# Performance work log

Hardware: AMD Instinct MI355X
Metric: run time of the kernel (lower is better)

The kernel has to match this reference:

```python
import jax, jax.numpy as jnp
import numpy as np

B, L, H, E = 2, 2048, 16, 64

def setup_inputs() -> dict:
    key = jax.random.key(0)
    kq, kk, kv = jax.random.split(key, 3)
    queries = jax.random.normal(kq, (B, L, H, E), dtype=jnp.float32)
    keys = jax.random.normal(kk, (B, L, H, E), dtype=jnp.float32)
    values = jax.random.normal(kv, (B, L, H, E), dtype=jnp.float32)
    # causal mask: True above the diagonal gets masked out (as in torch.triu(..., diagonal=1))
    attn_mask = jnp.broadcast_to(
        jnp.triu(jnp.ones((L, L), dtype=bool), k=1)[None, None, :, :], (B, 1, L, L)
    )
    return {"queries": queries, "keys": keys, "values": values, "attn_mask": attn_mask}

def reference(queries, keys, values, attn_mask):
    Ef = queries.shape[-1]
    # scores: [B, H, L, S]
    scores = jnp.einsum('blhe,bshe->bhls', queries, keys)
    scores = jnp.where(attn_mask, -jnp.inf, scores)
    # FAITHFUL to source: scale = 1/sqrt(E), then scores * (1.0/scale) = scores * sqrt(E)
    scale = 1.0 / jnp.sqrt(jnp.float32(Ef))
    attention_weights = jax.nn.softmax(scores * (1.0 / scale), axis=-1)
    # dropout p = 0.0 -> identity
    V = jnp.einsum('bhls,bshe->blhe', attention_weights, values)
    return V
```

## Files before the change

### kernel.cpp

```cpp
#include <hip/hip_runtime.h>

#define Bb 2
#define Ls 2048
#define Hh 16
#define Ee 64

#define QT 128
#define KT 64
#define BUFB 24576

typedef __fp16 f16;
typedef __attribute__((ext_vector_type(2)))  __fp16 f16x2;
typedef __attribute__((ext_vector_type(8)))  __fp16 f16x8;
typedef __attribute__((ext_vector_type(16))) float  f32x16;

union Frag  { f16x8 v; f16x2 h[4]; unsigned int u[4]; };
union U32H2 { f16x2 h; unsigned int u; };

__device__ __forceinline__ f16x2 pkrtz(float a, float b) {
  return __builtin_amdgcn_cvt_pkrtz(a, b);
}
__device__ __forceinline__ f32x16 mfma16(f16x8 a, f16x8 b, f32x16 c) {
  return __builtin_amdgcn_mfma_f32_32x32x16_f16(a, b, c, 0, 0, 0);
}
__device__ __forceinline__ f32x16 zero16() {
  f32x16 z;
#pragma unroll
  for (int i = 0; i < 16; ++i) z[i] = 0.f;
  return z;
}

#define SC 11.541560327111707f

__launch_bounds__(256, 2)
__global__ void fattn(const float* __restrict__ Q, const float* __restrict__ K,
                      const float* __restrict__ V, float* __restrict__ O) {
  __shared__ __align__(16) char lds[2 * BUFB];

  const int tid  = threadIdx.x;
  const int lane = tid & 63;
  const int wid  = tid >> 6;
  const int h2   = lane >> 5;
  const int qc   = lane & 31;
  const int bid  = blockIdx.x;

  const int bh  = bid & 31;
  const int qtx = bid >> 5;
  const int qt  = (qtx < 8) ? qtx : 23 - qtx;
  const int b   = bh >> 4;
  const int h   = bh & 15;

  const int q0   = qt * QT;
  const int q0w  = q0 + wid * 32;
  const int qrow = q0w + qc;

  f16x8 qh[4], ql[4];
  {
    const float* qp = Q + (((size_t)(b * Ls + qrow) * Hh) + h) * Ee + h2 * 8;
#pragma unroll
    for (int c = 0; c < 4; ++c) {
      float x[8];
      *(float4*)&x[0] = *(const float4*)(qp + c * 16);
      *(float4*)&x[4] = *(const float4*)(qp + c * 16 + 4);
      Frag fh, fl;
#pragma unroll
      for (int j = 0; j < 4; ++j) {
        f16x2 hi = pkrtz(x[2 * j], x[2 * j + 1]);
        fl.h[j] = pkrtz(x[2 * j] - (float)hi[0], x[2 * j + 1] - (float)hi[1]);
        fh.h[j] = hi;
      }
      qh[c] = fh.v;
      ql[c] = fl.v;
    }
  }

  const int r    = tid >> 2;
  const int cbe  = (tid & 3) * 16;
  const int kv0  = (tid & 31) * 2;
  const int ec   = tid >> 5;
  const float* kp0 = K + (((size_t)(b * Ls + r) * Hh) + h) * Ee + cbe;
  const float* vp0 = V + (((size_t)(b * Ls + kv0) * Hh) + h) * Ee + ec * 8;
  const int rowstride = Hh * Ee;

  float4 ka0, ka1, ka2, ka3, va0, va1, vb0, vb1;

#define STAGE_LOAD(KB)                                              \
  {                                                                 \
    const float* kp = kp0 + (size_t)(KB) * rowstride;               \
    ka0 = *(const float4*)(kp);                                     \
    ka1 = *(const float4*)(kp + 4);                                 \
    ka2 = *(const float4*)(kp + 8);                                 \
    ka3 = *(const float4*)(kp + 12);                                \
    const float* vp = vp0 + (size_t)(KB) * rowstride;               \
    va0 = *(const float4*)(vp);                                     \
    va1 = *(const float4*)(vp + 4);                                 \
    vb0 = *(const float4*)(vp + rowstride);                         \
    vb1 = *(const float4*)(vp + rowstride + 4);                     \
  }

#define STAGE_WRITE(BUF)                                            \
  {                                                                 \
    char* Khi = (BUF);                                              \
    char* Klo = (BUF) + 8192;                                       \
    char* Vt  = (BUF) + 16384;                                      \
    float x[16];                                                    \
    *(float4*)&x[0]  = ka0; *(float4*)&x[4]  = ka1;                 \
    *(float4*)&x[8]  = ka2; *(float4*)&x[12] = ka3;                 \
    Frag fh0, fl0, fh1, fl1;                                        \
    _Pragma("unroll")                                               \
    for (int j = 0; j < 4; ++j) {                                   \
      f16x2 hi0 = pkrtz(x[2 * j], x[2 * j + 1]);                    \
      fl0.h[j] = pkrtz(x[2 * j] - (float)hi0[0],                    \
                       x[2 * j + 1] - (float)hi0[1]);               \
      fh0.h[j] = hi0;                                               \
      f16x2 hi1 = pkrtz(x[8 + 2 * j], x[8 + 2 * j + 1]);            \
      fl1.h[j] = pkrtz(x[8 + 2 * j] - (float)hi1[0],                \
                       x[8 + 2 * j + 1] - (float)hi1[1]);           \
      fh1.h[j] = hi1;                                               \
    }                                                               \
    const int sw = (r & 7) << 4;                                    \
    char* dh = Khi + r * 128;                                       \
    char* dl = Klo + r * 128;                                       \
    *(f16x8*)(dh + ((cbe * 2) ^ sw))      = fh0.v;                  \
    *(f16x8*)(dh + ((cbe * 2 + 16) ^ sw)) = fh1.v;                  \
    *(f16x8*)(dl + ((cbe * 2) ^ sw))      = fl0.v;                  \
    *(f16x8*)(dl + ((cbe * 2 + 16) ^ sw)) = fl1.v;                  \
    float y0[8], y1[8];                                             \
    *(float4*)&y0[0] = va0; *(float4*)&y0[4] = va1;                 \
    *(float4*)&y1[0] = vb0; *(float4*)&y1[4] = vb1;                 \
    _Pragma("unroll")                                               \
    for (int j = 0; j < 8; ++j) {                                   \
      U32H2 pr;                                                     \
      pr.h = pkrtz(y0[j], y1[j]);                                   \
      const int e = ec * 8 + j;                                     \
      *(unsigned int*)(Vt + e * 128 + ((kv0 * 2) ^ ((e & 7) << 4))) = pr.u; \
    }                                                               \
  }

  f32x16 o0 = zero16(), o1 = zero16();
  float m = -3.0e38f, l = 0.f;

  const int NT = (q0 + QT) / KT;

  STAGE_LOAD(0);
  STAGE_WRITE(lds);
  __syncthreads();
  int cur = 0;

  for (int t = 0; t < NT; ++t) {
    const int kb = t * KT;
    const bool pf = (t + 1 < NT);
    if (pf) STAGE_LOAD(kb + KT);

    if (kb <= q0w + 31) {
      char* bufc = lds + cur * BUFB;
      char* Khi = bufc;
      char* Klo = bufc + 8192;
      char* Vt  = bufc + 16384;

      f32x16 s0, s1;
      {
        const int sw = (qc & 7) << 4;
        const char* kbh0 = Khi + qc * 128;
        const char* kbl0 = Klo + qc * 128;
        const char* kbh1 = Khi + (32 + qc) * 128;
        const char* kbl1 = Klo + (32 + qc) * 128;
        f32x16 a0h = zero16(), a0l = zero16(), a1h = zero16(), a1l = zero16();
        __builtin_amdgcn_s_setprio(1);
#pragma unroll
        for (int c = 0; c < 4; ++c) {
          const int off = ((c << 5) + (h2 << 4)) ^ sw;
          f16x8 ah0 = *(const f16x8*)(kbh0 + off);
          f16x8 al0 = *(const f16x8*)(kbl0 + off);
          f16x8 ah1 = *(const f16x8*)(kbh1 + off);
          f16x8 al1 = *(const f16x8*)(kbl1 + off);
          a0h = mfma16(ah0, qh[c], a0h);
          a1h = mfma16(ah1, qh[c], a1h);
          a0l = mfma16(ah0, ql[c], a0l);
          a1l = mfma16(ah1, ql[c], a1l);
          a0l = mfma16(al0, qh[c], a0l);
          a1l = mfma16(al1, qh[c], a1l);
        }
        __builtin_amdgcn_s_setprio(0);
#pragma unroll
        for (int i = 0; i < 16; ++i) { s0[i] = a0h[i] + a0l[i]; s1[i] = a1h[i] + a1l[i]; }
      }

      float p[32];
#pragma unroll
      for (int rr = 0; rr < 16; ++rr) { p[rr] = s0[rr]; p[16 + rr] = s1[rr]; }

      if (kb + KT - 1 > q0w) {
#pragma unroll
        for (int st = 0; st < 2; ++st)
#pragma unroll
          for (int rr = 0; rr < 16; ++rr) {
            const int kv = kb + st * 32 + ((rr & 3) + 8 * (rr >> 2) + 4 * h2);
            if (kv > qrow) p[st * 16 + rr] = -3.0e38f;
          }
      }

      float w[16];
#pragma unroll
      for (int i = 0; i < 16; ++i) w[i] = fmaxf(p[i], p[i + 16]);
#pragma unroll
      for (int i = 0; i < 8; ++i) w[i] = fmaxf(w[i], w[i + 8]);
#pragma unroll
      for (int i = 0; i < 4; ++i) w[i] = fmaxf(w[i], w[i + 4]);
      w[0] = fmaxf(fmaxf(w[0], w[1]), fmaxf(w[2], w[3]));
      float tm = fmaxf(w[0], __shfl_xor(w[0], 32));

      if (__any(tm > m + 1.0f)) {
        const float mnew = fmaxf(m, tm);
        const float corr = __builtin_amdgcn_exp2f((m - mnew) * SC);
        l *= corr;
#pragma unroll
        for (int rr = 0; rr < 16; ++rr) {
          const float cr = __shfl(corr, (rr & 3) + 8 * (rr >> 2) + 4 * h2);
          o0[rr] *= cr;
          o1[rr] *= cr;
        }
        m = mnew;
      }
      const float base = m * SC;
#pragma unroll
      for (int i = 0; i < 32; ++i) p[i] = __builtin_amdgcn_exp2f(p[i] * SC - base);
      float z[16];
#pragma unroll
      for (int i = 0; i < 16; ++i) z[i] = p[i] + p[i + 16];
#pragma unroll
      for (int i = 0; i < 8; ++i) z[i] += z[i + 8];
#pragma unroll
      for (int i = 0; i < 4; ++i) z[i] += z[i + 4];
      float ps = (z[0] + z[1]) + (z[2] + z[3]);
      ps += __shfl_xor(ps, 32);
      l += ps;

      f16x8 pa[4];
#pragma unroll
      for (int st = 0; st < 2; ++st) {
        unsigned u[8];
#pragma unroll
        for (int g = 0; g < 4; ++g) {
          U32H2 a, bb;
          a.h  = pkrtz(p[st * 16 + 4 * g],     p[st * 16 + 4 * g + 1]);
          bb.h = pkrtz(p[st * 16 + 4 * g + 2], p[st * 16 + 4 * g + 3]);
          u[2 * g]     = a.u;
          u[2 * g + 1] = bb.u;
        }
#pragma unroll
        for (int cp = 0; cp < 2; ++cp) {
          const unsigned ua0 = u[4 * cp], ua1 = u[4 * cp + 1];
          const unsigned ub0 = u[4 * cp + 2], ub1 = u[4 * cp + 3];
          const unsigned t0 = (unsigned)__shfl_xor((int)(h2 ? ua0 : ub0), 32);
          const unsigned t1 = (unsigned)__shfl_xor((int)(h2 ? ua1 : ub1), 32);
          Frag f;
          f.u[0] = h2 ? t0 : ua0;
          f.u[1] = h2 ? t1 : ua1;
          f.u[2] = h2 ? ub0 : t0;
          f.u[3] = h2 ? ub1 : t1;
          pa[st * 2 + cp] = f.v;
        }
      }

      {
        const int sw = (qc & 7) << 4;
        __builtin_amdgcn_s_setprio(1);
#pragma unroll
        for (int c = 0; c < 4; ++c) {
          const int off = ((c << 5) + (h2 << 4)) ^ sw;
          const f16x8 vbl0 = *(const f16x8*)(Vt + (qc)      * 128 + off);
          const f16x8 vbl1 = *(const f16x8*)(Vt + (32 + qc) * 128 + off);
          o0 = mfma16(pa[c], vbl0, o0);
          o1 = mfma16(pa[c], vbl1, o1);
        }
        __builtin_amdgcn_s_setprio(0);
      }
    }

    if (pf) STAGE_WRITE(lds + (cur ^ 1) * BUFB);
    __syncthreads();
    cur ^= 1;
  }

  const float inv = 1.0f / l;
#pragma unroll
  for (int rr = 0; rr < 16; ++rr) {
    const int row = (rr & 3) + 8 * (rr >> 2) + 4 * h2;
    const float iv = __shfl(inv, row);
    float* op = O + (((size_t)(b * Ls + q0w + row) * Hh) + h) * Ee;
    op[qc]      = o0[rr] * iv;
    op[32 + qc] = o1[rr] * iv;
  }
}

extern "C" void kernel_launch(void* const* d_in, const int* in_sizes, int n_in,
                              void* d_out, int out_size, void* d_ws, size_t ws_size,
                              hipStream_t stream) {
  const float* Q = (const float*)d_in[0];
  const float* K = (const float*)d_in[1];
  const float* V = (const float*)d_in[2];
  float* O = (float*)d_out;
  (void)in_sizes; (void)n_in; (void)out_size; (void)d_ws; (void)ws_size;
  dim3 grid(Bb * Hh * (Ls / QT));
  fattn<<<grid, dim3(256), 0, stream>>>(Q, K, V, O);
}
```

Measured before the change: 164.8 us.

## Switch to 16x16x32 MFMA tiles with 8 waves of 16 query rows

```diff
diff --git a/kernel.cpp b/kernel.cpp
--- a/kernel.cpp
+++ b/kernel.cpp
@@ -10,9 +10,9 @@
 #define BUFB 24576
 
 typedef __fp16 f16;
-typedef __attribute__((ext_vector_type(2)))  __fp16 f16x2;
-typedef __attribute__((ext_vector_type(8)))  __fp16 f16x8;
-typedef __attribute__((ext_vector_type(16))) float  f32x16;
+typedef __attribute__((ext_vector_type(2))) __fp16 f16x2;
+typedef __attribute__((ext_vector_type(8))) __fp16 f16x8;
+typedef __attribute__((ext_vector_type(4))) float  f32x4;
 
 union Frag  { f16x8 v; f16x2 h[4]; unsigned int u[4]; };
 union U32H2 { f16x2 h; unsigned int u; };
@@ -20,19 +20,13 @@
 __device__ __forceinline__ f16x2 pkrtz(float a, float b) {
   return __builtin_amdgcn_cvt_pkrtz(a, b);
 }
-__device__ __forceinline__ f32x16 mfma16(f16x8 a, f16x8 b, f32x16 c) {
-  return __builtin_amdgcn_mfma_f32_32x32x16_f16(a, b, c, 0, 0, 0);
-}
-__device__ __forceinline__ f32x16 zero16() {
-  f32x16 z;
-#pragma unroll
-  for (int i = 0; i < 16; ++i) z[i] = 0.f;
-  return z;
+__device__ __forceinline__ f32x4 mfma16(f16x8 a, f16x8 b, f32x4 c) {
+  return __builtin_amdgcn_mfma_f32_16x16x32_f16(a, b, c, 0, 0, 0);
 }
 
 #define SC 11.541560327111707f
 
-__launch_bounds__(256, 2)
+__launch_bounds__(512, 4)
 __global__ void fattn(const float* __restrict__ Q, const float* __restrict__ K,
                       const float* __restrict__ V, float* __restrict__ O) {
   __shared__ __align__(16) char lds[2 * BUFB];
@@ -40,8 +34,8 @@
   const int tid  = threadIdx.x;
   const int lane = tid & 63;
   const int wid  = tid >> 6;
-  const int h2   = lane >> 5;
-  const int qc   = lane & 31;
+  const int g    = lane >> 4;
+  const int q15  = lane & 15;
   const int bid  = blockIdx.x;
 
   const int bh  = bid & 31;
@@ -51,17 +45,17 @@
   const int h   = bh & 15;
 
   const int q0   = qt * QT;
-  const int q0w  = q0 + wid * 32;
-  const int qrow = q0w + qc;
-
-  f16x8 qh[4], ql[4];
+  const int q0w  = q0 + wid * 16;
+  const int qrow = q0w + q15;
+
+  f16x8 qh[2], ql[2];
   {
-    const float* qp = Q + (((size_t)(b * Ls + qrow) * Hh) + h) * Ee + h2 * 8;
-#pragma unroll
-    for (int c = 0; c < 4; ++c) {
+    const float* qp = Q + (((size_t)(b * Ls + qrow) * Hh) + h) * Ee + 8 * g;
+#pragma unroll
+    for (int c = 0; c < 2; ++c) {
       float x[8];
-      *(float4*)&x[0] = *(const float4*)(qp + c * 16);
-      *(float4*)&x[4] = *(const float4*)(qp + c * 16 + 4);
+      *(float4*)&x[0] = *(const float4*)(qp + 32 * c);
+      *(float4*)&x[4] = *(const float4*)(qp + 32 * c + 4);
       Frag fh, fl;
 #pragma unroll
       for (int j = 0; j < 4; ++j) {
@@ -74,208 +68,189 @@
     }
   }
 
-  const int r    = tid >> 2;
-  const int cbe  = (tid & 3) * 16;
+  const int r    = tid >> 3;
+  const int cbe  = (tid & 7) * 8;
   const int kv0  = (tid & 31) * 2;
-  const int ec   = tid >> 5;
+  const int ec4  = (tid >> 5) * 4;
   const float* kp0 = K + (((size_t)(b * Ls + r) * Hh) + h) * Ee + cbe;
-  const float* vp0 = V + (((size_t)(b * Ls + kv0) * Hh) + h) * Ee + ec * 8;
+  const float* vp0 = V + (((size_t)(b * Ls + kv0) * Hh) + h) * Ee + ec4;
   const int rowstride = Hh * Ee;
 
-  float4 ka0, ka1, ka2, ka3, va0, va1, vb0, vb1;
-
-#define STAGE_LOAD(KB)                                              \
-  {                                                                 \
-    const float* kp = kp0 + (size_t)(KB) * rowstride;               \
-    ka0 = *(const float4*)(kp);                                     \
-    ka1 = *(const float4*)(kp + 4);                                 \
-    ka2 = *(const float4*)(kp + 8);                                 \
-    ka3 = *(const float4*)(kp + 12);                                \
-    const float* vp = vp0 + (size_t)(KB) * rowstride;               \
-    va0 = *(const float4*)(vp);                                     \
-    va1 = *(const float4*)(vp + 4);                                 \
-    vb0 = *(const float4*)(vp + rowstride);                         \
-    vb1 = *(const float4*)(vp + rowstride + 4);                     \
-  }
-
-#define STAGE_WRITE(BUF)                                            \
-  {                                                                 \
-    char* Khi = (BUF);                                              \
-    char* Klo = (BUF) + 8192;                                       \
-    char* Vt  = (BUF) + 16384;                                      \
-    float x[16];                                                    \
-    *(float4*)&x[0]  = ka0; *(float4*)&x[4]  = ka1;                 \
-    *(float4*)&x[8]  = ka2; *(float4*)&x[12] = ka3;                 \
-    Frag fh0, fl0, fh1, fl1;                                        \
-    _Pragma("unroll")                                               \
-    for (int j = 0; j < 4; ++j) {                                   \
-      f16x2 hi0 = pkrtz(x[2 * j], x[2 * j + 1]);                    \
-      fl0.h[j] = pkrtz(x[2 * j] - (float)hi0[0],                    \
-                       x[2 * j + 1] - (float)hi0[1]);               \
-      fh0.h[j] = hi0;                                               \
-      f16x2 hi1 = pkrtz(x[8 + 2 * j], x[8 + 2 * j + 1]);            \
-      fl1.h[j] = pkrtz(x[8 + 2 * j] - (float)hi1[0],                \
-                       x[8 + 2 * j + 1] - (float)hi1[1]);           \
-      fh1.h[j] = hi1;                                               \
-    }                                                               \
-    const int sw = (r & 7) << 4;                                    \
-    char* dh = Khi + r * 128;                                       \
-    char* dl = Klo + r * 128;                                       \
-    *(f16x8*)(dh + ((cbe * 2) ^ sw))      = fh0.v;                  \
-    *(f16x8*)(dh + ((cbe * 2 + 16) ^ sw)) = fh1.v;                  \
-    *(f16x8*)(dl + ((cbe * 2) ^ sw))      = fl0.v;                  \
-    *(f16x8*)(dl + ((cbe * 2 + 16) ^ sw)) = fl1.v;                  \
-    float y0[8], y1[8];                                             \
-    *(float4*)&y0[0] = va0; *(float4*)&y0[4] = va1;                 \
-    *(float4*)&y1[0] = vb0; *(float4*)&y1[4] = vb1;                 \
-    _Pragma("unroll")                                               \
-    for (int j = 0; j < 8; ++j) {                                   \
-      U32H2 pr;                                                     \
-      pr.h = pkrtz(y0[j], y1[j]);                                   \
-      const int e = ec * 8 + j;                                     \
+  float4 ka0, ka1, va0, vb0;
+
+#define STAGE_LOAD(KB)                                          \
+  {                                                             \
+    const float* kp = kp0 + (size_t)(KB) * rowstride;           \
+    ka0 = *(const float4*)(kp);                                 \
+    ka1 = *(const float4*)(kp + 4);                             \
+    const float* vp = vp0 + (size_t)(KB) * rowstride;           \
+    va0 = *(const float4*)(vp);                                 \
+    vb0 = *(const float4*)(vp + rowstride);                     \
+  }
+
+#define STAGE_WRITE(BUF)                                        \
+  {                                                             \
+    char* Khi = (BUF);                                          \
+    char* Klo = (BUF) + 8192;                                   \
+    char* Vt  = (BUF) + 16384;                                  \
+    float x[8];                                                 \
+    *(float4*)&x[0] = ka0; *(float4*)&x[4] = ka1;               \
+    Frag fh, fl;                                                \
+    _Pragma("unroll")                                           \
+    for (int j = 0; j < 4; ++j) {                               \
+      f16x2 hi = pkrtz(x[2 * j], x[2 * j + 1]);                 \
+      fl.h[j] = pkrtz(x[2 * j] - (float)hi[0],                  \
+                      x[2 * j + 1] - (float)hi[1]);             \
+      fh.h[j] = hi;                                             \
+    }                                                           \
+    const int sw = (r & 7) << 4;                                \
+    *(f16x8*)(Khi + r * 128 + ((cbe * 2) ^ sw)) = fh.v;         \
+    *(f16x8*)(Klo + r * 128 + ((cbe * 2) ^ sw)) = fl.v;         \
+    _Pragma("unroll")                                           \
+    for (int j = 0; j < 4; ++j) {                               \
+      U32H2 pr;                                                 \
+      pr.h = pkrtz(va0[j], vb0[j]);                             \
+      const int e = ec4 + j;                                    \
       *(unsigned int*)(Vt + e * 128 + ((kv0 * 2) ^ ((e & 7) << 4))) = pr.u; \
-    }                                                               \
-  }
-
-  f32x16 o0 = zero16(), o1 = zero16();
+    }                                                           \
+  }
+
+  f32x4 o0, o1, o2, o3;
+#pragma unroll
+  for (int i = 0; i < 4; ++i) { o0[i] = 0.f; o1[i] = 0.f; o2[i] = 0.f; o3[i] = 0.f; }
   float m = -3.0e38f, l = 0.f;
 
-  const int NT = (q0 + QT) / KT;
+  const int NT = 2 * (qt + 1);
 
   STAGE_LOAD(0);
   STAGE_WRITE(lds);
   __syncthreads();
   int cur = 0;
 
+  const int swr   = (q15 & 7) << 4;
+  const int srcA  = q15 + ((g & 1) ? 32 : 0);
+  const int srcB  = srcA + 16;
+  const int srel  = g >> 1;
+  const int lbase = lane & 48;
+
   for (int t = 0; t < NT; ++t) {
     const int kb = t * KT;
     const bool pf = (t + 1 < NT);
     if (pf) STAGE_LOAD(kb + KT);
 
-    if (kb <= q0w + 31) {
+    if (kb <= q0w + 15) {
       char* bufc = lds + cur * BUFB;
       char* Khi = bufc;
       char* Klo = bufc + 8192;
       char* Vt  = bufc + 16384;
 
-      f32x16 s0, s1;
-      {
-        const int sw = (qc & 7) << 4;
-        const char* kbh0 = Khi + qc * 128;
-        const char* kbl0 = Klo + qc * 128;
-        const char* kbh1 = Khi + (32 + qc) * 128;
-        const char* kbl1 = Klo + (32 + qc) * 128;
-        f32x16 a0h = zero16(), a0l = zero16(), a1h = zero16(), a1l = zero16();
-        __builtin_amdgcn_s_setprio(1);
-#pragma unroll
-        for (int c = 0; c < 4; ++c) {
-          const int off = ((c << 5) + (h2 << 4)) ^ sw;
-          f16x8 ah0 = *(const f16x8*)(kbh0 + off);
-          f16x8 al0 = *(const f16x8*)(kbl0 + off);
-          f16x8 ah1 = *(const f16x8*)(kbh1 + off);
-          f16x8 al1 = *(const f16x8*)(kbl1 + off);
-          a0h = mfma16(ah0, qh[c], a0h);
-          a1h = mfma16(ah1, qh[c], a1h);
-          a0l = mfma16(ah0, ql[c], a0l);
-          a1l = mfma16(ah1, ql[c], a1l);
-          a0l = mfma16(al0, qh[c], a0l);
-          a1l = mfma16(al1, qh[c], a1l);
+      f32x4 p4[4];
+      __builtin_amdgcn_s_setprio(1);
+#pragma unroll
+      for (int st = 0; st < 4; ++st) {
+        const char* kh = Khi + (16 * st + q15) * 128;
+        const char* kl = Klo + (16 * st + q15) * 128;
+        f32x4 acch, accl;
+#pragma unroll
+        for (int i = 0; i < 4; ++i) { acch[i] = 0.f; accl[i] = 0.f; }
+#pragma unroll
+        for (int c = 0; c < 2; ++c) {
+          const int off = ((c << 6) + (g << 4)) ^ swr;
+          f16x8 ah = *(const f16x8*)(kh + off);
+          f16x8 al = *(const f16x8*)(kl + off);
+          acch = mfma16(ah, qh[c], acch);
+          accl = mfma16(ah, ql[c], accl);
+          accl = mfma16(al, qh[c], accl);
         }
-        __builtin_amdgcn_s_setprio(0);
-#pragma unroll
-        for (int i = 0; i < 16; ++i) { s0[i] = a0h[i] + a0l[i]; s1[i] = a1h[i] + a1l[i]; }
-      }
-
-      float p[32];
-#pragma unroll
-      for (int rr = 0; rr < 16; ++rr) { p[rr] = s0[rr]; p[16 + rr] = s1[rr]; }
+        p4[st] = acch + accl;
+      }
+      __builtin_amdgcn_s_setprio(0);
 
       if (kb + KT - 1 > q0w) {
 #pragma unroll
-        for (int st = 0; st < 2; ++st)
-#pragma unroll
-          for (int rr = 0; rr < 16; ++rr) {
-            const int kv = kb + st * 32 + ((rr & 3) + 8 * (rr >> 2) + 4 * h2);
-            if (kv > qrow) p[st * 16 + rr] = -3.0e38f;
+        for (int st = 0; st < 4; ++st)
+#pragma unroll
+          for (int rg = 0; rg < 4; ++rg) {
+            const int kv = kb + 16 * st + 4 * g + rg;
+            if (kv > qrow) p4[st][rg] = -3.0e38f;
           }
       }
 
-      float w[16];
-#pragma unroll
-      for (int i = 0; i < 16; ++i) w[i] = fmaxf(p[i], p[i + 16]);
-#pragma unroll
-      for (int i = 0; i < 8; ++i) w[i] = fmaxf(w[i], w[i + 8]);
-#pragma unroll
-      for (int i = 0; i < 4; ++i) w[i] = fmaxf(w[i], w[i + 4]);
-      w[0] = fmaxf(fmaxf(w[0], w[1]), fmaxf(w[2], w[3]));
-      float tm = fmaxf(w[0], __shfl_xor(w[0], 32));
+      f32x4 tv = p4[0];
+#pragma unroll
+      for (int i = 0; i < 4; ++i) tv[i] = fmaxf(fmaxf(p4[0][i], p4[1][i]), fmaxf(p4[2][i], p4[3][i]));
+      float tm = fmaxf(fmaxf(tv[0], tv[1]), fmaxf(tv[2], tv[3]));
+      tm = fmaxf(tm, __shfl_xor(tm, 16));
+      tm = fmaxf(tm, __shfl_xor(tm, 32));
 
       if (__any(tm > m + 1.0f)) {
         const float mnew = fmaxf(m, tm);
         const float corr = __builtin_amdgcn_exp2f((m - mnew) * SC);
         l *= corr;
 #pragma unroll
-        for (int rr = 0; rr < 16; ++rr) {
-          const float cr = __shfl(corr, (rr & 3) + 8 * (rr >> 2) + 4 * h2);
-          o0[rr] *= cr;
-          o1[rr] *= cr;
+        for (int rg = 0; rg < 4; ++rg) {
+          const float cr = __shfl(corr, lbase | (4 * g + rg));
+          o0[rg] *= cr; o1[rg] *= cr; o2[rg] *= cr; o3[rg] *= cr;
         }
         m = mnew;
       }
       const float base = m * SC;
 #pragma unroll
-      for (int i = 0; i < 32; ++i) p[i] = __builtin_amdgcn_exp2f(p[i] * SC - base);
-      float z[16];
-#pragma unroll
-      for (int i = 0; i < 16; ++i) z[i] = p[i] + p[i + 16];
-#pragma unroll
-      for (int i = 0; i < 8; ++i) z[i] += z[i + 8];
-#pragma unroll
-      for (int i = 0; i < 4; ++i) z[i] += z[i + 4];
-      float ps = (z[0] + z[1]) + (z[2] + z[3]);
-      ps += __shfl_xor(ps, 32);
-      l += ps;
-
-      f16x8 pa[4];
-#pragma unroll
-      for (int st = 0; st < 2; ++st) {
-        unsigned u[8];
-#pragma unroll
-        for (int g = 0; g < 4; ++g) {
-          U32H2 a, bb;
-          a.h  = pkrtz(p[st * 16 + 4 * g],     p[st * 16 + 4 * g + 1]);
-          bb.h = pkrtz(p[st * 16 + 4 * g + 2], p[st * 16 + 4 * g + 3]);
-          u[2 * g]     = a.u;
-          u[2 * g + 1] = bb.u;
-        }
-#pragma unroll
-        for (int cp = 0; cp < 2; ++cp) {
-          const unsigned ua0 = u[4 * cp], ua1 = u[4 * cp + 1];
-          const unsigned ub0 = u[4 * cp + 2], ub1 = u[4 * cp + 3];
-          const unsigned t0 = (unsigned)__shfl_xor((int)(h2 ? ua0 : ub0), 32);
-          const unsigned t1 = (unsigned)__shfl_xor((int)(h2 ? ua1 : ub1), 32);
-          Frag f;
-          f.u[0] = h2 ? t0 : ua0;
-          f.u[1] = h2 ? t1 : ua1;
-          f.u[2] = h2 ? ub0 : t0;
-          f.u[3] = h2 ? ub1 : t1;
-          pa[st * 2 + cp] = f.v;
-        }
-      }
+      for (int st = 0; st < 4; ++st)
+#pragma unroll
+        for (int rg = 0; rg < 4; ++rg)
+          p4[st][rg] = __builtin_amdgcn_exp2f(p4[st][rg] * SC - base);
 
       {
-        const int sw = (qc & 7) << 4;
-        __builtin_amdgcn_s_setprio(1);
-#pragma unroll
-        for (int c = 0; c < 4; ++c) {
-          const int off = ((c << 5) + (h2 << 4)) ^ sw;
-          const f16x8 vbl0 = *(const f16x8*)(Vt + (qc)      * 128 + off);
-          const f16x8 vbl1 = *(const f16x8*)(Vt + (32 + qc) * 128 + off);
-          o0 = mfma16(pa[c], vbl0, o0);
-          o1 = mfma16(pa[c], vbl1, o1);
-        }
-        __builtin_amdgcn_s_setprio(0);
-      }
+        f32x4 sv = (p4[0] + p4[1]) + (p4[2] + p4[3]);
+        float ps = (sv[0] + sv[1]) + (sv[2] + sv[3]);
+        ps += __shfl_xor(ps, 16);
+        ps += __shfl_xor(ps, 32);
+        l += ps;
+      }
+
+      unsigned int u[8];
+#pragma unroll
+      for (int st = 0; st < 4; ++st) {
+        U32H2 w0, w1;
+        w0.h = pkrtz(p4[st][0], p4[st][1]);
+        w1.h = pkrtz(p4[st][2], p4[st][3]);
+        u[2 * st]     = w0.u;
+        u[2 * st + 1] = w1.u;
+      }
+      f16x8 pa[2];
+#pragma unroll
+      for (int c = 0; c < 2; ++c) {
+        const unsigned a0 = (unsigned)__shfl((int)u[4 * c + 0], srcA);
+        const unsigned a1 = (unsigned)__shfl((int)u[4 * c + 1], srcA);
+        const unsigned a2 = (unsigned)__shfl((int)u[4 * c + 0], srcB);
+        const unsigned a3 = (unsigned)__shfl((int)u[4 * c + 1], srcB);
+        const unsigned b0 = (unsigned)__shfl((int)u[4 * c + 2], srcA);
+        const unsigned b1 = (unsigned)__shfl((int)u[4 * c + 3], srcA);
+        const unsigned b2 = (unsigned)__shfl((int)u[4 * c + 2], srcB);
+        const unsigned b3 = (unsigned)__shfl((int)u[4 * c + 3], srcB);
+        Frag f;
+        f.u[0] = srel ? b0 : a0;
+        f.u[1] = srel ? b1 : a1;
+        f.u[2] = srel ? b2 : a2;
+        f.u[3] = srel ? b3 : a3;
+        pa[c] = f.v;
+      }
+
+      __builtin_amdgcn_s_setprio(1);
+#pragma unroll
+      for (int c = 0; c < 2; ++c) {
+        const int coff = ((c << 6) + (g << 4)) ^ swr;
+        const f16x8 v0 = *(const f16x8*)(Vt + (q15)      * 128 + coff);
+        const f16x8 v1 = *(const f16x8*)(Vt + (16 + q15) * 128 + coff);
+        const f16x8 v2 = *(const f16x8*)(Vt + (32 + q15) * 128 + coff);
+        const f16x8 v3 = *(const f16x8*)(Vt + (48 + q15) * 128 + coff);
+        o0 = mfma16(pa[c], v0, o0);
+        o1 = mfma16(pa[c], v1, o1);
+        o2 = mfma16(pa[c], v2, o2);
+        o3 = mfma16(pa[c], v3, o3);
+      }
+      __builtin_amdgcn_s_setprio(0);
     }
 
     if (pf) STAGE_WRITE(lds + (cur ^ 1) * BUFB);
@@ -285,12 +260,13 @@
 
   const float inv = 1.0f / l;
 #pragma unroll
-  for (int rr = 0; rr < 16; ++rr) {
-    const int row = (rr & 3) + 8 * (rr >> 2) + 4 * h2;
-    const float iv = __shfl(inv, row);
-    float* op = O + (((size_t)(b * Ls + q0w + row) * Hh) + h) * Ee;
-    op[qc]      = o0[rr] * iv;
-    op[32 + qc] = o1[rr] * iv;
+  for (int rg = 0; rg < 4; ++rg) {
+    const float iv = __shfl(inv, lbase | (4 * g + rg));
+    float* op = O + (((size_t)(b * Ls + q0w + 4 * g + rg) * Hh) + h) * Ee + q15;
+    op[0]  = o0[rg] * iv;
+    op[16] = o1[rg] * iv;
+    op[32] = o2[rg] * iv;
+    op[48] = o3[rg] * iv;
   }
 }
 
@@ -302,6 +278,5 @@
   const float* V = (const float*)d_in[2];
   float* O = (float*)d_out;
   (void)in_sizes; (void)n_in; (void)out_size; (void)d_ws; (void)ws_size;
-  dim3 grid(Bb * Hh * (Ls / QT));
-  fattn<<<grid, dim3(256), 0, stream>>>(Q, K, V, O);
-}
+  fattn<<<dim3(Bb * Hh * (Ls / QT)), dim3(512), 0, stream>>>(Q, K, V, O);
+}
```

New measurement: 164.3 us. About the same (-0.3%).

## Software-pipeline QK^T one tile ahead and transpose PV output layout

Applied to the files above, without the earlier changes.

```diff
diff --git a/kernel.cpp b/kernel.cpp
--- a/kernel.cpp
+++ b/kernel.cpp
@@ -10,8 +10,8 @@
 #define BUFB 24576
 
 typedef __fp16 f16;
-typedef __attribute__((ext_vector_type(2)))  __fp16 f16x2;
-typedef __attribute__((ext_vector_type(8)))  __fp16 f16x8;
+typedef __attribute__((ext_vector_type(2))) __fp16 f16x2;
+typedef __attribute__((ext_vector_type(8))) __fp16 f16x8;
 typedef __attribute__((ext_vector_type(16))) float  f32x16;
 
 union Frag  { f16x8 v; f16x2 h[4]; unsigned int u[4]; };
@@ -20,7 +20,7 @@
 __device__ __forceinline__ f16x2 pkrtz(float a, float b) {
   return __builtin_amdgcn_cvt_pkrtz(a, b);
 }
-__device__ __forceinline__ f32x16 mfma16(f16x8 a, f16x8 b, f32x16 c) {
+__device__ __forceinline__ f32x16 mfma32(f16x8 a, f16x8 b, f32x16 c) {
   return __builtin_amdgcn_mfma_f32_32x32x16_f16(a, b, c, 0, 0, 0);
 }
 __device__ __forceinline__ f32x16 zero16() {
@@ -31,6 +31,28 @@
 }
 
 #define SC 11.541560327111707f
+
+#define QKT(BUF, S0, S1)                                          \
+  {                                                               \
+    const char* Khi_ = (BUF);                                     \
+    const char* Klo_ = (BUF) + 8192;                              \
+    _Pragma("unroll")                                             \
+    for (int st_ = 0; st_ < 2; ++st_) {                           \
+      const char* kh_ = Khi_ + (32 * st_ + qc) * 128;             \
+      const char* kl_ = Klo_ + (32 * st_ + qc) * 128;             \
+      f32x16 acch_ = zero16(), accl_ = zero16();                  \
+      _Pragma("unroll")                                           \
+      for (int c_ = 0; c_ < 4; ++c_) {                            \
+        const int off_ = ((c_ << 5) + (h2 << 4)) ^ swr;           \
+        f16x8 ah_ = *(const f16x8*)(kh_ + off_);                  \
+        f16x8 al_ = *(const f16x8*)(kl_ + off_);                  \
+        acch_ = mfma32(ah_, qh[c_], acch_);                       \
+        accl_ = mfma32(ah_, ql[c_], accl_);                       \
+        accl_ = mfma32(al_, qh[c_], accl_);                       \
+      }                                                           \
+      if (st_) S1 = acch_ + accl_; else S0 = acch_ + accl_;       \
+    }                                                             \
+  }
 
 __launch_bounds__(256, 2)
 __global__ void fattn(const float* __restrict__ Q, const float* __restrict__ K,
@@ -53,6 +75,7 @@
   const int q0   = qt * QT;
   const int q0w  = q0 + wid * 32;
   const int qrow = q0w + qc;
+  const int swr  = (qc & 7) << 4;
 
   f16x8 qh[4], ql[4];
   {
@@ -140,157 +163,128 @@
   f32x16 o0 = zero16(), o1 = zero16();
   float m = -3.0e38f, l = 0.f;
 
-  const int NT = (q0 + QT) / KT;
+  const int NT = 2 * (qt + 1);
 
   STAGE_LOAD(0);
   STAGE_WRITE(lds);
   __syncthreads();
-  int cur = 0;
+  STAGE_LOAD(KT);
+  f32x16 s0, s1;
+  QKT(lds, s0, s1);
+  STAGE_WRITE(lds + BUFB);
+  __syncthreads();
 
   for (int t = 0; t < NT; ++t) {
     const int kb = t * KT;
-    const bool pf = (t + 1 < NT);
-    if (pf) STAGE_LOAD(kb + KT);
-
+    char* cbuf = lds + (t & 1) * BUFB;
+    char* nbuf = lds + ((t + 1) & 1) * BUFB;
+    const bool pf2 = (t + 2 < NT);
+    if (pf2) STAGE_LOAD(kb + 2 * KT);
+
+    f32x16 n0 = s0, n1 = s1;
     if (kb <= q0w + 31) {
-      char* bufc = lds + cur * BUFB;
-      char* Khi = bufc;
-      char* Klo = bufc + 8192;
-      char* Vt  = bufc + 16384;
-
-      f32x16 s0, s1;
-      {
-        const int sw = (qc & 7) << 4;
-        const char* kbh0 = Khi + qc * 128;
-        const char* kbl0 = Klo + qc * 128;
-        const char* kbh1 = Khi + (32 + qc) * 128;
-        const char* kbl1 = Klo + (32 + qc) * 128;
-        f32x16 a0h = zero16(), a0l = zero16(), a1h = zero16(), a1l = zero16();
-        __builtin_amdgcn_s_setprio(1);
-#pragma unroll
-        for (int c = 0; c < 4; ++c) {
-          const int off = ((c << 5) + (h2 << 4)) ^ sw;
-          f16x8 ah0 = *(const f16x8*)(kbh0 + off);
-          f16x8 al0 = *(const f16x8*)(kbl0 + off);
-          f16x8 ah1 = *(const f16x8*)(kbh1 + off);
-          f16x8 al1 = *(const f16x8*)(kbl1 + off);
-          a0h = mfma16(ah0, qh[c], a0h);
-          a1h = mfma16(ah1, qh[c], a1h);
-          a0l = mfma16(ah0, ql[c], a0l);
-          a1l = mfma16(ah1, ql[c], a1l);
-          a0l = mfma16(al0, qh[c], a0l);
-          a1l = mfma16(al1, qh[c], a1l);
-        }
-        __builtin_amdgcn_s_setprio(0);
-#pragma unroll
-        for (int i = 0; i < 16; ++i) { s0[i] = a0h[i] + a0l[i]; s1[i] = a1h[i] + a1l[i]; }
-      }
+      __builtin_amdgcn_s_setprio(1);
+      QKT(nbuf, n0, n1);
 
       float p[32];
 #pragma unroll
       for (int rr = 0; rr < 16; ++rr) { p[rr] = s0[rr]; p[16 + rr] = s1[rr]; }
-
       if (kb + KT - 1 > q0w) {
 #pragma unroll
         for (int st = 0; st < 2; ++st)
 #pragma unroll
           for (int rr = 0; rr < 16; ++rr) {
-            const int kv = kb + st * 32 + ((rr & 3) + 8 * (rr >> 2) + 4 * h2);
+            const int kv = kb + 32 * st + ((rr & 3) + 8 * (rr >> 2) + 4 * h2);
             if (kv > qrow) p[st * 16 + rr] = -3.0e38f;
           }
       }
-
-      float w[16];
-#pragma unroll
-      for (int i = 0; i < 16; ++i) w[i] = fmaxf(p[i], p[i + 16]);
-#pragma unroll
-      for (int i = 0; i < 8; ++i) w[i] = fmaxf(w[i], w[i + 8]);
+      float w[8];
+#pragma unroll
+      for (int i = 0; i < 8; ++i) w[i] = fmaxf(fmaxf(p[i], p[i + 8]), fmaxf(p[i + 16], p[i + 24]));
 #pragma unroll
       for (int i = 0; i < 4; ++i) w[i] = fmaxf(w[i], w[i + 4]);
-      w[0] = fmaxf(fmaxf(w[0], w[1]), fmaxf(w[2], w[3]));
-      float tm = fmaxf(w[0], __shfl_xor(w[0], 32));
+      float tm = fmaxf(fmaxf(w[0], w[1]), fmaxf(w[2], w[3]));
+      tm = fmaxf(tm, __shfl_xor(tm, 32));
 
       if (__any(tm > m + 1.0f)) {
         const float mnew = fmaxf(m, tm);
         const float corr = __builtin_amdgcn_exp2f((m - mnew) * SC);
         l *= corr;
 #pragma unroll
-        for (int rr = 0; rr < 16; ++rr) {
-          const float cr = __shfl(corr, (rr & 3) + 8 * (rr >> 2) + 4 * h2);
-          o0[rr] *= cr;
-          o1[rr] *= cr;
+        for (int i = 0; i < 16; ++i) { o0[i] *= corr; o1[i] *= corr; }
+        m = mnew;
+      }
+      const float base = m * SC;
+#pragma unroll
+      for (int i = 0; i < 32; ++i) p[i] = __builtin_amdgcn_exp2f(p[i] * SC - base);
+      {
+        float z[8];
+#pragma unroll
+        for (int i = 0; i < 8; ++i) z[i] = (p[i] + p[i + 8]) + (p[i + 16] + p[i + 24]);
+#pragma unroll
+        for (int i = 0; i < 4; ++i) z[i] += z[i + 4];
+        float ps = (z[0] + z[1]) + (z[2] + z[3]);
+        ps += __shfl_xor(ps, 32);
+        l += ps;
+      }
+
+      Frag pb[2][2];
+#pragma unroll
+      for (int st = 0; st < 2; ++st) {
+        unsigned pk[8];
+#pragma unroll
+        for (int j = 0; j < 8; ++j) {
+          U32H2 t2;
+          t2.h = pkrtz(p[st * 16 + 2 * j], p[st * 16 + 2 * j + 1]);
+          pk[j] = t2.u;
         }
-        m = mnew;
-      }
-      const float base = m * SC;
-#pragma unroll
-      for (int i = 0; i < 32; ++i) p[i] = __builtin_amdgcn_exp2f(p[i] * SC - base);
-      float z[16];
-#pragma unroll
-      for (int i = 0; i < 16; ++i) z[i] = p[i] + p[i + 16];
-#pragma unroll
-      for (int i = 0; i < 8; ++i) z[i] += z[i + 8];
-#pragma unroll
-      for (int i = 0; i < 4; ++i) z[i] += z[i + 4];
-      float ps = (z[0] + z[1]) + (z[2] + z[3]);
-      ps += __shfl_xor(ps, 32);
-      l += ps;
-
-      f16x8 pa[4];
-#pragma unroll
-      for (int st = 0; st < 2; ++st) {
-        unsigned u[8];
-#pragma unroll
-        for (int g = 0; g < 4; ++g) {
-          U32H2 a, bb;
-          a.h  = pkrtz(p[st * 16 + 4 * g],     p[st * 16 + 4 * g + 1]);
-          bb.h = pkrtz(p[st * 16 + 4 * g + 2], p[st * 16 + 4 * g + 3]);
-          u[2 * g]     = a.u;
-          u[2 * g + 1] = bb.u;
-        }
-#pragma unroll
-        for (int cp = 0; cp < 2; ++cp) {
-          const unsigned ua0 = u[4 * cp], ua1 = u[4 * cp + 1];
-          const unsigned ub0 = u[4 * cp + 2], ub1 = u[4 * cp + 3];
-          const unsigned t0 = (unsigned)__shfl_xor((int)(h2 ? ua0 : ub0), 32);
-          const unsigned t1 = (unsigned)__shfl_xor((int)(h2 ? ua1 : ub1), 32);
-          Frag f;
-          f.u[0] = h2 ? t0 : ua0;
-          f.u[1] = h2 ? t1 : ua1;
-          f.u[2] = h2 ? ub0 : t0;
-          f.u[3] = h2 ? ub1 : t1;
-          pa[st * 2 + cp] = f.v;
-        }
+        const unsigned r0 = (unsigned)__shfl_xor((int)(h2 ? pk[0] : pk[2]), 32);
+        const unsigned r1 = (unsigned)__shfl_xor((int)(h2 ? pk[1] : pk[3]), 32);
+        const unsigned r2 = (unsigned)__shfl_xor((int)(h2 ? pk[4] : pk[6]), 32);
+        const unsigned r3 = (unsigned)__shfl_xor((int)(h2 ? pk[5] : pk[7]), 32);
+        pb[st][0].u[0] = h2 ? r0 : pk[0];
+        pb[st][0].u[1] = h2 ? r1 : pk[1];
+        pb[st][0].u[2] = h2 ? pk[2] : r0;
+        pb[st][0].u[3] = h2 ? pk[3] : r1;
+        pb[st][1].u[0] = h2 ? r2 : pk[4];
+        pb[st][1].u[1] = h2 ? r3 : pk[5];
+        pb[st][1].u[2] = h2 ? pk[6] : r2;
+        pb[st][1].u[3] = h2 ? pk[7] : r3;
       }
 
       {
-        const int sw = (qc & 7) << 4;
-        __builtin_amdgcn_s_setprio(1);
-#pragma unroll
-        for (int c = 0; c < 4; ++c) {
-          const int off = ((c << 5) + (h2 << 4)) ^ sw;
-          const f16x8 vbl0 = *(const f16x8*)(Vt + (qc)      * 128 + off);
-          const f16x8 vbl1 = *(const f16x8*)(Vt + (32 + qc) * 128 + off);
-          o0 = mfma16(pa[c], vbl0, o0);
-          o1 = mfma16(pa[c], vbl1, o1);
-        }
-        __builtin_amdgcn_s_setprio(0);
-      }
+        const char* Vt = cbuf + 16384;
+#pragma unroll
+        for (int st = 0; st < 2; ++st)
+#pragma unroll
+          for (int c2 = 0; c2 < 2; ++c2) {
+            const int off = (64 * st + 32 * c2 + 16 * h2) ^ swr;
+            const f16x8 va = *(const f16x8*)(Vt + qc * 128 + off);
+            const f16x8 vb = *(const f16x8*)(Vt + (32 + qc) * 128 + off);
+            o0 = mfma32(va, pb[st][c2].v, o0);
+            o1 = mfma32(vb, pb[st][c2].v, o1);
+          }
+      }
+      __builtin_amdgcn_s_setprio(0);
     }
 
-    if (pf) STAGE_WRITE(lds + (cur ^ 1) * BUFB);
     __syncthreads();
-    cur ^= 1;
+    if (pf2) STAGE_WRITE(cbuf);
+    __syncthreads();
+    s0 = n0; s1 = n1;
   }
 
   const float inv = 1.0f / l;
-#pragma unroll
-  for (int rr = 0; rr < 16; ++rr) {
-    const int row = (rr & 3) + 8 * (rr >> 2) + 4 * h2;
-    const float iv = __shfl(inv, row);
-    float* op = O + (((size_t)(b * Ls + q0w + row) * Hh) + h) * Ee;
-    op[qc]      = o0[rr] * iv;
-    op[32 + qc] = o1[rr] * iv;
+  float* op = O + (((size_t)(b * Ls + qrow) * Hh) + h) * Ee;
+#pragma unroll
+  for (int j = 0; j < 4; ++j) {
+    float4 w0, w1;
+    w0.x = o0[4 * j] * inv;     w0.y = o0[4 * j + 1] * inv;
+    w0.z = o0[4 * j + 2] * inv; w0.w = o0[4 * j + 3] * inv;
+    w1.x = o1[4 * j] * inv;     w1.y = o1[4 * j + 1] * inv;
+    w1.z = o1[4 * j + 2] * inv; w1.w = o1[4 * j + 3] * inv;
+    *(float4*)(op + 8 * j + 4 * h2)      = w0;
+    *(float4*)(op + 32 + 8 * j + 4 * h2) = w1;
   }
 }
 
@@ -302,6 +296,5 @@
   const float* V = (const float*)d_in[2];
   float* O = (float*)d_out;
   (void)in_sizes; (void)n_in; (void)out_size; (void)d_ws; (void)ws_size;
-  dim3 grid(Bb * Hh * (Ls / QT));
-  fattn<<<grid, dim3(256), 0, stream>>>(Q, K, V, O);
-}
+  fattn<<<dim3(Bb * Hh * (Ls / QT)), dim3(256), 0, stream>>>(Q, K, V, O);
+}
```

Measured after the change: 161.0 us. 2.3% less time.
